# Optimization experiments

Hardware: AMD Instinct MI355X
Metric: run time of the kernel (lower is better)

The kernel has to match this reference:

```python
import jax, jax.numpy as jnp
import numpy as np

MODES1 = 32
MODES2 = 32


def _dct1_last(x):
    # Unnormalized DCT-I along last axis via rfft of even-symmetric extension.
    # For length N input, extension [x0..x_{N-1}, x_{N-2}..x_1] has length 2(N-1);
    # rfft yields N real coefficients == scipy.fftpack.dct(x, type=1).
    ext = jnp.concatenate([x, x[..., -2:0:-1]], axis=-1)
    return jnp.fft.rfft(ext, axis=-1).real.astype(x.dtype)


def _dct1_2d(x):
    # DCT-I along last two axes (separable). scipy idct type-1 (unnormalized)
    # is identical to dct type-1, so this serves as both dctn and idctn.
    x = _dct1_last(x)
    x = jnp.swapaxes(x, -1, -2)
    x = _dct1_last(x)
    return jnp.swapaxes(x, -1, -2)


def setup_inputs() -> dict:
    key = jax.random.key(0)
    k1, k2, k3 = jax.random.split(key, 3)
    B, Cin, Cout, H, W = 8, 64, 64, 256, 256
    scale = 1.0 / (Cin * Cout)
    x = jax.random.normal(k1, (B, Cin, H, W), dtype=jnp.float32)
    weights1 = scale * jax.random.uniform(k2, (Cin, Cout, MODES1, MODES2), dtype=jnp.float32)
    weights2 = scale * jax.random.uniform(k3, (Cin, Cout, MODES1, MODES2), dtype=jnp.float32)
    return {"x": x, "weights1": weights1, "weights2": weights2}


def reference(x, weights1, weights2):
    B, Cin, H, W = x.shape
    Cout = weights1.shape[1]
    Wh = W // 2 + 1  # width of truncated spectral tensor (torch used cfloat, imag==0)
    m1, m2 = MODES1, MODES2

    x_dct = _dct1_2d(x)  # [B, Cin, H, W]

    low = jnp.einsum('bixy,ioxy->boxy', x_dct[:, :, :m1, :m2], weights1)
    high = jnp.einsum('bixy,ioxy->boxy', x_dct[:, :, -m1:, :m2], weights2)

    out_ft = jnp.zeros((B, Cout, H, Wh), dtype=x.dtype)
    out_ft = out_ft.at[:, :, :m1, :m2].set(low)
    out_ft = out_ft.at[:, :, H - m1:, :m2].set(high)

    # idctn(..., type=1, shape=(H, W)) zero-pads the last axis from Wh to W,
    # then applies unnormalized IDCT-I == DCT-I along axes 2,3.
    out_full = jnp.pad(out_ft, ((0, 0), (0, 0), (0, 0), (0, W - Wh)))
    return _dct1_2d(out_full)
```

## Files before the change

kernel.cpp:

```cpp
#include <hip/hip_runtime.h>
#include <math.h>

#define OFF_AT  0
#define OFF_BMT 16384
#define OFF_CMT 24576
#define OFF_DMT 40960
#define OFF_Y   49152
#define OFF_Z   1097728

__device__ __forceinline__ float cosT(int p) {
    int r = p % 510;
    if (r > 255) r = 510 - r;
    return cosf((float)r * (3.14159265358979323846f / 255.0f));
}

__global__ __launch_bounds__(256) void init_basis(float* __restrict__ ws) {
    int idx = blockIdx.x * 256 + threadIdx.x;
    if (idx < 16384) {
        int h = idx >> 6, r = idx & 63;
        int k1 = (r < 32) ? r : r + 192;
        float we = (h == 0 || h == 255) ? 1.f : 2.f;
        ws[OFF_AT + idx] = we * cosT(k1 * h);
    } else if (idx < 24576) {
        int j = idx - 16384; int w = j >> 5, y = j & 31;
        float we = (w == 0 || w == 255) ? 1.f : 2.f;
        ws[OFF_BMT + j] = we * cosT(y * w);
    } else if (idx < 40960) {
        int j = idx - 24576; int r = j >> 8, h = j & 255;
        int k1 = (r < 32) ? r : r + 192;
        float wsl = (r == 0 || r == 63) ? 1.f : 2.f;
        ws[OFF_CMT + j] = wsl * cosT(k1 * h);
    } else if (idx < 49152) {
        int j = idx - 40960; int y = j >> 8, w = j & 255;
        float wy = (y == 0) ? 1.f : 2.f;
        ws[OFF_DMT + j] = wy * cosT(y * w);
    }
}

__global__ __launch_bounds__(256) void fwd_kernel(const float* __restrict__ x,
                                                  const float* __restrict__ ws,
                                                  float* __restrict__ Y) {
    __shared__ float buf[9216];
    __shared__ float bmt[1024];
    const int t = threadIdx.x;
    const int bi = blockIdx.x;
    const float* xp = x + (size_t)bi * 65536;
    const int l = t & 63;
    const int y8 = (t >> 6) * 8;

    float acc[4][8];
#pragma unroll
    for (int j = 0; j < 4; ++j)
#pragma unroll
        for (int yy = 0; yy < 8; ++yy) acc[j][yy] = 0.f;

    const int colv = (t & 7) * 4;
    const int rbase = t >> 3;

    for (int c = 0; c < 8; ++c) {
#pragma unroll
        for (int r = 0; r < 8; ++r) {
            int row = r * 32 + rbase;
            float4 v = *(const float4*)(xp + row * 256 + c * 32 + colv);
            float* dst = &buf[row * 33 + colv];
            dst[0] = v.x; dst[1] = v.y; dst[2] = v.z; dst[3] = v.w;
        }
        {
            int wloc = t >> 3;
            int y4 = (t & 7) * 4;
            *(float4*)&bmt[wloc * 32 + y4] =
                *(const float4*)(ws + OFF_BMT + (c * 32 + wloc) * 32 + y4);
        }
        __syncthreads();
#pragma unroll 8
        for (int w = 0; w < 32; ++w) {
            float xv0 = buf[l * 33 + w];
            float xv1 = buf[(l + 64) * 33 + w];
            float xv2 = buf[(l + 128) * 33 + w];
            float xv3 = buf[(l + 192) * 33 + w];
            float4 b0 = *(float4*)&bmt[w * 32 + y8];
            float4 b1 = *(float4*)&bmt[w * 32 + y8 + 4];
            float bv[8] = {b0.x, b0.y, b0.z, b0.w, b1.x, b1.y, b1.z, b1.w};
#pragma unroll
            for (int yy = 0; yy < 8; ++yy) {
                acc[0][yy] += xv0 * bv[yy];
                acc[1][yy] += xv1 * bv[yy];
                acc[2][yy] += xv2 * bv[yy];
                acc[3][yy] += xv3 * bv[yy];
            }
        }
        __syncthreads();
    }
#pragma unroll
    for (int j = 0; j < 4; ++j)
#pragma unroll
        for (int yy = 0; yy < 8; ++yy)
            buf[(l + 64 * j) * 36 + y8 + yy] = acc[j][yy];
    __syncthreads();

    float acc2[8];
#pragma unroll
    for (int yy = 0; yy < 8; ++yy) acc2[yy] = 0.f;
    const float* At = ws + OFF_AT;
#pragma unroll 4
    for (int h = 0; h < 256; ++h) {
        float av = At[h * 64 + l];
        float4 t0 = *(float4*)&buf[h * 36 + y8];
        float4 t1 = *(float4*)&buf[h * 36 + y8 + 4];
        acc2[0] += av * t0.x; acc2[1] += av * t0.y;
        acc2[2] += av * t0.z; acc2[3] += av * t0.w;
        acc2[4] += av * t1.x; acc2[5] += av * t1.y;
        acc2[6] += av * t1.z; acc2[7] += av * t1.w;
    }
    float* Yp = Y + (size_t)bi * 2048 + l * 32 + y8;
    *(float4*)Yp       = make_float4(acc2[0], acc2[1], acc2[2], acc2[3]);
    *(float4*)(Yp + 4) = make_float4(acc2[4], acc2[5], acc2[6], acc2[7]);
}

__global__ __launch_bounds__(256) void mix_kernel(const float* __restrict__ w1,
                                                  const float* __restrict__ w2,
                                                  const float* __restrict__ Yv,
                                                  float* __restrict__ Z) {
    const int xp = blockIdx.x & 63;
    const int o0 = (blockIdx.x >> 6) * 16;
    const int t = threadIdx.x;
    const int yh = t & 15;
    const int oo = t >> 4;
    const int o = o0 + oo;
    const int y = yh * 2;

    const float* Wbase = (xp < 32) ? (w1 + xp * 32) : (w2 + (xp - 32) * 32);
    Wbase += o * 1024 + y;
    const float* Yb = Yv + xp * 32 + y;

    float acc[8][2];
#pragma unroll
    for (int b = 0; b < 8; ++b) { acc[b][0] = 0.f; acc[b][1] = 0.f; }

    for (int i = 0; i < 64; ++i) {
        float2 wv = *(const float2*)(Wbase + i * 65536);
#pragma unroll
        for (int b = 0; b < 8; ++b) {
            float2 yv = *(const float2*)(Yb + (b * 64 + i) * 2048);
            acc[b][0] += yv.x * wv.x;
            acc[b][1] += yv.y * wv.y;
        }
    }
#pragma unroll
    for (int b = 0; b < 8; ++b) {
        float2 r; r.x = acc[b][0]; r.y = acc[b][1];
        *(float2*)(Z + (size_t)(b * 64 + o) * 2048 + xp * 32 + y) = r;
    }
}

__global__ __launch_bounds__(256) void inv_kernel(const float* __restrict__ ws,
                                                  const float* __restrict__ Zv,
                                                  float* __restrict__ out) {
    __shared__ float zs[2048];
    __shared__ float dmts[8192];
    __shared__ float t2t[4224];
    const int t = threadIdx.x;
    const int bo = blockIdx.x;
    const float* Zp = Zv + (size_t)bo * 2048;
    float* op = out + (size_t)bo * 65536;

    *(float4*)&zs[t * 8]     = *(const float4*)(Zp + t * 8);
    *(float4*)&zs[t * 8 + 4] = *(const float4*)(Zp + t * 8 + 4);
#pragma unroll
    for (int k = 0; k < 8; ++k)
        *(float4*)&dmts[k * 1024 + t * 4] =
            *(const float4*)(ws + OFF_DMT + k * 1024 + t * 4);
    __syncthreads();

    const int l6 = t & 63;
    const int y8 = (t >> 6) * 8;
    const int l5 = t & 31;
    const int j  = t >> 5;

    for (int hh = 0; hh < 2; ++hh) {
        float a1[2][8];
#pragma unroll
        for (int jj = 0; jj < 2; ++jj)
#pragma unroll
            for (int yy = 0; yy < 8; ++yy) a1[jj][yy] = 0.f;
        const float* Cm = ws + OFF_CMT + hh * 128 + l6;
#pragma unroll 4
        for (int xpi = 0; xpi < 64; ++xpi) {
            float av0 = Cm[xpi * 256];
            float av1 = Cm[xpi * 256 + 64];
            float4 z0 = *(float4*)&zs[xpi * 32 + y8];
            float4 z1 = *(float4*)&zs[xpi * 32 + y8 + 4];
            float zv[8] = {z0.x, z0.y, z0.z, z0.w, z1.x, z1.y, z1.z, z1.w};
#pragma unroll
            for (int yy = 0; yy < 8; ++yy) {
                a1[0][yy] += av0 * zv[yy];
                a1[1][yy] += av1 * zv[yy];
            }
        }
#pragma unroll
        for (int jj = 0; jj < 2; ++jj)
#pragma unroll
            for (int yy = 0; yy < 8; ++yy)
                t2t[(y8 + yy) * 132 + l6 + 64 * jj] = a1[jj][yy];
        __syncthreads();

        for (int hg = 0; hg < 2; ++hg) {
            float a2[8][8];
#pragma unroll
            for (int ii = 0; ii < 8; ++ii)
#pragma unroll
                for (int ww = 0; ww < 8; ++ww) a2[ii][ww] = 0.f;
            const int hb = hg * 64 + j * 8;
#pragma unroll 4
            for (int y = 0; y < 32; ++y) {
                float4 ta = *(float4*)&t2t[y * 132 + hb];
                float4 tb = *(float4*)&t2t[y * 132 + hb + 4];
                float4 da = *(float4*)&dmts[y * 256 + l5 * 8];
                float4 db = *(float4*)&dmts[y * 256 + l5 * 8 + 4];
                float tv[8] = {ta.x, ta.y, ta.z, ta.w, tb.x, tb.y, tb.z, tb.w};
                float dv[8] = {da.x, da.y, da.z, da.w, db.x, db.y, db.z, db.w};
#pragma unroll
                for (int ii = 0; ii < 8; ++ii)
#pragma unroll
                    for (int ww = 0; ww < 8; ++ww)
                        a2[ii][ww] += tv[ii] * dv[ww];
            }
#pragma unroll
            for (int ii = 0; ii < 8; ++ii) {
                int h = hh * 128 + hb + ii;
                float* o8 = op + h * 256 + l5 * 8;
                *(float4*)o8       = make_float4(a2[ii][0], a2[ii][1], a2[ii][2], a2[ii][3]);
                *(float4*)(o8 + 4) = make_float4(a2[ii][4], a2[ii][5], a2[ii][6], a2[ii][7]);
            }
        }
        __syncthreads();
    }
}

extern "C" void kernel_launch(void* const* d_in, const int* in_sizes, int n_in,
                              void* d_out, int out_size, void* d_ws, size_t ws_size,
                              hipStream_t stream) {
    const float* x  = (const float*)d_in[0];
    const float* w1 = (const float*)d_in[1];
    const float* w2 = (const float*)d_in[2];
    float* out = (float*)d_out;
    float* ws  = (float*)d_ws;

    hipLaunchKernelGGL(init_basis, dim3(192), dim3(256), 0, stream, ws);
    hipLaunchKernelGGL(fwd_kernel, dim3(512), dim3(256), 0, stream, x, ws, ws + OFF_Y);
    hipLaunchKernelGGL(mix_kernel, dim3(256), dim3(256), 0, stream, w1, w2,
                       ws + OFF_Y, ws + OFF_Z);
    hipLaunchKernelGGL(inv_kernel, dim3(512), dim3(256), 0, stream, ws, ws + OFF_Z, out);
}
```

Baseline: 326.8 us.

## Double-buffer forward stage, widen blocks to 512 threads, split mix work finer

The forward kernel now streams 16-column chunks of the input through double-buffered LDS with an XOR swizzle, prefetching the next chunk into registers while computing the current one, and uses 512 threads per block. The inverse kernel also moves to 512 threads, handling both h-groups in one pass instead of looping. The mix kernel is split across four times as many blocks, each thread covering two batches instead of eight, for more parallelism. This aims to raise occupancy and hide global memory latency, at the cost of less per-thread reuse and more redundant weight loads in the mix stage.

```diff
diff --git a/kernel.cpp b/kernel.cpp
--- a/kernel.cpp
+++ b/kernel.cpp
@@ -37,125 +37,129 @@
     }
 }
 
-__global__ __launch_bounds__(256) void fwd_kernel(const float* __restrict__ x,
-                                                  const float* __restrict__ ws,
-                                                  float* __restrict__ Y) {
-    __shared__ float buf[9216];
-    __shared__ float bmt[1024];
+__global__ __launch_bounds__(512, 4) void fwd_kernel(const float* __restrict__ x,
+                                                     const float* __restrict__ ws,
+                                                     float* __restrict__ Y) {
+    __shared__ float lds[9216];
     const int t = threadIdx.x;
     const int bi = blockIdx.x;
     const float* xp = x + (size_t)bi * 65536;
-    const int l = t & 63;
-    const int y8 = (t >> 6) * 8;
-
-    float acc[4][8];
-#pragma unroll
-    for (int j = 0; j < 4; ++j)
+
+    const int srow = t >> 2;
+    const int scol = (t & 3) * 4;
+    const int scolz = scol ^ (4 * ((srow >> 1) & 3));
+
+    const int hb = t & 127;
+    const int y8 = (t >> 7) * 8;
+    const int csw = 4 * ((hb >> 1) & 3);
+
+    float acc[2][8];
+#pragma unroll
+    for (int j = 0; j < 2; ++j)
 #pragma unroll
         for (int yy = 0; yy < 8; ++yy) acc[j][yy] = 0.f;
 
-    const int colv = (t & 7) * 4;
-    const int rbase = t >> 3;
-
-    for (int c = 0; c < 8; ++c) {
-#pragma unroll
-        for (int r = 0; r < 8; ++r) {
-            int row = r * 32 + rbase;
-            float4 v = *(const float4*)(xp + row * 256 + c * 32 + colv);
-            float* dst = &buf[row * 33 + colv];
-            dst[0] = v.x; dst[1] = v.y; dst[2] = v.z; dst[3] = v.w;
-        }
-        {
-            int wloc = t >> 3;
-            int y4 = (t & 7) * 4;
-            *(float4*)&bmt[wloc * 32 + y4] =
-                *(const float4*)(ws + OFF_BMT + (c * 32 + wloc) * 32 + y4);
+    float4 sx0 = *(const float4*)(xp + srow * 256 + scol);
+    float4 sx1 = *(const float4*)(xp + (srow + 128) * 256 + scol);
+    float  sb  = ws[OFF_BMT + t];
+    *(float4*)&lds[srow * 16 + scolz] = sx0;
+    *(float4*)&lds[(srow + 128) * 16 + scolz] = sx1;
+    lds[8192 + t] = sb;
+    __syncthreads();
+
+    for (int c = 0; c < 16; ++c) {
+        const int cur = c & 1;
+        if (c < 15) {
+            const int wofs = (c + 1) * 16;
+            sx0 = *(const float4*)(xp + srow * 256 + wofs + scol);
+            sx1 = *(const float4*)(xp + (srow + 128) * 256 + wofs + scol);
+            sb  = ws[OFF_BMT + (c + 1) * 512 + t];
+        }
+        const float* xs = lds + cur * 4096;
+        const float* bs = lds + 8192 + cur * 512;
+#pragma unroll
+        for (int w = 0; w < 16; w += 4) {
+            const int wz = w ^ csw;
+            float4 xa = *(const float4*)&xs[hb * 16 + wz];
+            float4 xc = *(const float4*)&xs[(hb + 128) * 16 + wz];
+            const float xav[4] = {xa.x, xa.y, xa.z, xa.w};
+            const float xcv[4] = {xc.x, xc.y, xc.z, xc.w};
+#pragma unroll
+            for (int k = 0; k < 4; ++k) {
+                float4 b0 = *(const float4*)&bs[(w + k) * 32 + y8];
+                float4 b1 = *(const float4*)&bs[(w + k) * 32 + y8 + 4];
+                const float bv[8] = {b0.x, b0.y, b0.z, b0.w, b1.x, b1.y, b1.z, b1.w};
+#pragma unroll
+                for (int yy = 0; yy < 8; ++yy) {
+                    acc[0][yy] += xav[k] * bv[yy];
+                    acc[1][yy] += xcv[k] * bv[yy];
+                }
+            }
+        }
+        if (c < 15) {
+            const int nxt = cur ^ 1;
+            *(float4*)&lds[nxt * 4096 + srow * 16 + scolz] = sx0;
+            *(float4*)&lds[nxt * 4096 + (srow + 128) * 16 + scolz] = sx1;
+            lds[8192 + nxt * 512 + t] = sb;
         }
         __syncthreads();
-#pragma unroll 8
-        for (int w = 0; w < 32; ++w) {
-            float xv0 = buf[l * 33 + w];
-            float xv1 = buf[(l + 64) * 33 + w];
-            float xv2 = buf[(l + 128) * 33 + w];
-            float xv3 = buf[(l + 192) * 33 + w];
-            float4 b0 = *(float4*)&bmt[w * 32 + y8];
-            float4 b1 = *(float4*)&bmt[w * 32 + y8 + 4];
-            float bv[8] = {b0.x, b0.y, b0.z, b0.w, b1.x, b1.y, b1.z, b1.w};
-#pragma unroll
-            for (int yy = 0; yy < 8; ++yy) {
-                acc[0][yy] += xv0 * bv[yy];
-                acc[1][yy] += xv1 * bv[yy];
-                acc[2][yy] += xv2 * bv[yy];
-                acc[3][yy] += xv3 * bv[yy];
-            }
-        }
-        __syncthreads();
-    }
-#pragma unroll
-    for (int j = 0; j < 4; ++j)
-#pragma unroll
-        for (int yy = 0; yy < 8; ++yy)
-            buf[(l + 64 * j) * 36 + y8 + yy] = acc[j][yy];
+    }
+
+#pragma unroll
+    for (int j = 0; j < 2; ++j) {
+        const int row = hb + 128 * j;
+        *(float4*)&lds[row * 36 + y8]     = make_float4(acc[j][0], acc[j][1], acc[j][2], acc[j][3]);
+        *(float4*)&lds[row * 36 + y8 + 4] = make_float4(acc[j][4], acc[j][5], acc[j][6], acc[j][7]);
+    }
     __syncthreads();
 
-    float acc2[8];
-#pragma unroll
-    for (int yy = 0; yy < 8; ++yy) acc2[yy] = 0.f;
+    const int r2 = t & 63;
+    const int y4 = (t >> 6) * 4;
+    float a2[4] = {0.f, 0.f, 0.f, 0.f};
     const float* At = ws + OFF_AT;
 #pragma unroll 4
     for (int h = 0; h < 256; ++h) {
-        float av = At[h * 64 + l];
-        float4 t0 = *(float4*)&buf[h * 36 + y8];
-        float4 t1 = *(float4*)&buf[h * 36 + y8 + 4];
-        acc2[0] += av * t0.x; acc2[1] += av * t0.y;
-        acc2[2] += av * t0.z; acc2[3] += av * t0.w;
-        acc2[4] += av * t1.x; acc2[5] += av * t1.y;
-        acc2[6] += av * t1.z; acc2[7] += av * t1.w;
-    }
-    float* Yp = Y + (size_t)bi * 2048 + l * 32 + y8;
-    *(float4*)Yp       = make_float4(acc2[0], acc2[1], acc2[2], acc2[3]);
-    *(float4*)(Yp + 4) = make_float4(acc2[4], acc2[5], acc2[6], acc2[7]);
+        const float av = At[h * 64 + r2];
+        const float4 tv = *(const float4*)&lds[h * 36 + y4];
+        a2[0] += av * tv.x; a2[1] += av * tv.y; a2[2] += av * tv.z; a2[3] += av * tv.w;
+    }
+    float* Yp = Y + (size_t)bi * 2048 + r2 * 32 + y4;
+    *(float4*)Yp = make_float4(a2[0], a2[1], a2[2], a2[3]);
 }
 
 __global__ __launch_bounds__(256) void mix_kernel(const float* __restrict__ w1,
                                                   const float* __restrict__ w2,
                                                   const float* __restrict__ Yv,
                                                   float* __restrict__ Z) {
-    const int xp = blockIdx.x & 63;
-    const int o0 = (blockIdx.x >> 6) * 16;
-    const int t = threadIdx.x;
-    const int yh = t & 15;
-    const int oo = t >> 4;
-    const int o = o0 + oo;
-    const int y = yh * 2;
-
-    const float* Wbase = (xp < 32) ? (w1 + xp * 32) : (w2 + (xp - 32) * 32);
-    Wbase += o * 1024 + y;
-    const float* Yb = Yv + xp * 32 + y;
-
-    float acc[8][2];
-#pragma unroll
-    for (int b = 0; b < 8; ++b) { acc[b][0] = 0.f; acc[b][1] = 0.f; }
-
+    const int r  = blockIdx.x & 63;
+    const int og = blockIdx.x >> 6;
+    const int t  = threadIdx.x;
+    const int y  = (t & 15) * 2;
+    const int o  = og * 4 + ((t >> 4) & 3);
+    const int bp = t >> 6;
+
+    const float* Wb = ((r < 32) ? (w1 + r * 32) : (w2 + (r - 32) * 32)) + o * 1024 + y;
+    const float* Y0 = Yv + (size_t)(bp * 64) * 2048 + r * 32 + y;
+    const float* Y1 = Y0 + (size_t)4 * 64 * 2048;
+
+    float a00 = 0.f, a01 = 0.f, a10 = 0.f, a11 = 0.f;
+#pragma unroll 4
     for (int i = 0; i < 64; ++i) {
-        float2 wv = *(const float2*)(Wbase + i * 65536);
-#pragma unroll
-        for (int b = 0; b < 8; ++b) {
-            float2 yv = *(const float2*)(Yb + (b * 64 + i) * 2048);
-            acc[b][0] += yv.x * wv.x;
-            acc[b][1] += yv.y * wv.y;
-        }
-    }
-#pragma unroll
-    for (int b = 0; b < 8; ++b) {
-        float2 r; r.x = acc[b][0]; r.y = acc[b][1];
-        *(float2*)(Z + (size_t)(b * 64 + o) * 2048 + xp * 32 + y) = r;
-    }
-}
-
-__global__ __launch_bounds__(256) void inv_kernel(const float* __restrict__ ws,
-                                                  const float* __restrict__ Zv,
-                                                  float* __restrict__ out) {
+        const float2 wv = *(const float2*)(Wb + (size_t)i * 65536);
+        const float2 p  = *(const float2*)(Y0 + i * 2048);
+        const float2 q  = *(const float2*)(Y1 + i * 2048);
+        a00 += p.x * wv.x; a01 += p.y * wv.y;
+        a10 += q.x * wv.x; a11 += q.y * wv.y;
+    }
+    float2 r0; r0.x = a00; r0.y = a01;
+    float2 r1; r1.x = a10; r1.y = a11;
+    *(float2*)(Z + (size_t)(bp * 64 + o) * 2048 + r * 32 + y) = r0;
+    *(float2*)(Z + (size_t)((bp + 4) * 64 + o) * 2048 + r * 32 + y) = r1;
+}
+
+__global__ __launch_bounds__(512, 4) void inv_kernel(const float* __restrict__ ws,
+                                                     const float* __restrict__ Zv,
+                                                     float* __restrict__ out) {
     __shared__ float zs[2048];
     __shared__ float dmts[8192];
     __shared__ float t2t[4224];
@@ -164,74 +168,66 @@
     const float* Zp = Zv + (size_t)bo * 2048;
     float* op = out + (size_t)bo * 65536;
 
-    *(float4*)&zs[t * 8]     = *(const float4*)(Zp + t * 8);
-    *(float4*)&zs[t * 8 + 4] = *(const float4*)(Zp + t * 8 + 4);
-#pragma unroll
-    for (int k = 0; k < 8; ++k)
-        *(float4*)&dmts[k * 1024 + t * 4] =
-            *(const float4*)(ws + OFF_DMT + k * 1024 + t * 4);
+    *(float4*)&zs[t * 4] = *(const float4*)(Zp + t * 4);
+#pragma unroll
+    for (int k = 0; k < 4; ++k)
+        *(float4*)&dmts[k * 2048 + t * 4] = *(const float4*)(ws + OFF_DMT + k * 2048 + t * 4);
     __syncthreads();
 
-    const int l6 = t & 63;
-    const int y8 = (t >> 6) * 8;
-    const int l5 = t & 31;
-    const int j  = t >> 5;
+    const int hb = t & 63;
+    const int y4 = (t >> 6) * 4;
+    const int wl = t & 31;
+    const int hg = t >> 5;
+    const int w0 = wl * 8;
 
     for (int hh = 0; hh < 2; ++hh) {
-        float a1[2][8];
-#pragma unroll
-        for (int jj = 0; jj < 2; ++jj)
-#pragma unroll
-            for (int yy = 0; yy < 8; ++yy) a1[jj][yy] = 0.f;
-        const float* Cm = ws + OFF_CMT + hh * 128 + l6;
+        float a1[2][4];
+#pragma unroll
+        for (int j = 0; j < 2; ++j)
+#pragma unroll
+            for (int k = 0; k < 4; ++k) a1[j][k] = 0.f;
+        const float* Cm = ws + OFF_CMT + hh * 128 + hb;
+#pragma unroll 2
+        for (int r = 0; r < 64; ++r) {
+            const float4 zv = *(const float4*)&zs[r * 32 + y4];
+            const float av0 = Cm[r * 256];
+            const float av1 = Cm[r * 256 + 64];
+            a1[0][0] += av0 * zv.x; a1[0][1] += av0 * zv.y; a1[0][2] += av0 * zv.z; a1[0][3] += av0 * zv.w;
+            a1[1][0] += av1 * zv.x; a1[1][1] += av1 * zv.y; a1[1][2] += av1 * zv.z; a1[1][3] += av1 * zv.w;
+        }
+#pragma unroll
+        for (int j = 0; j < 2; ++j)
+#pragma unroll
+            for (int k = 0; k < 4; ++k)
+                t2t[(y4 + k) * 132 + hb + 64 * j] = a1[j][k];
+        __syncthreads();
+
+        const int hbl = hg * 8;
+        float a2[8][8];
+#pragma unroll
+        for (int ii = 0; ii < 8; ++ii)
+#pragma unroll
+            for (int ww = 0; ww < 8; ++ww) a2[ii][ww] = 0.f;
 #pragma unroll 4
-        for (int xpi = 0; xpi < 64; ++xpi) {
-            float av0 = Cm[xpi * 256];
-            float av1 = Cm[xpi * 256 + 64];
-            float4 z0 = *(float4*)&zs[xpi * 32 + y8];
-            float4 z1 = *(float4*)&zs[xpi * 32 + y8 + 4];
-            float zv[8] = {z0.x, z0.y, z0.z, z0.w, z1.x, z1.y, z1.z, z1.w};
-#pragma unroll
-            for (int yy = 0; yy < 8; ++yy) {
-                a1[0][yy] += av0 * zv[yy];
-                a1[1][yy] += av1 * zv[yy];
-            }
-        }
-#pragma unroll
-        for (int jj = 0; jj < 2; ++jj)
-#pragma unroll
-            for (int yy = 0; yy < 8; ++yy)
-                t2t[(y8 + yy) * 132 + l6 + 64 * jj] = a1[jj][yy];
-        __syncthreads();
-
-        for (int hg = 0; hg < 2; ++hg) {
-            float a2[8][8];
+        for (int y = 0; y < 32; ++y) {
+            const float4 ta = *(const float4*)&t2t[y * 132 + hbl];
+            const float4 tb = *(const float4*)&t2t[y * 132 + hbl + 4];
+            const float4 da = *(const float4*)&dmts[y * 256 + w0];
+            const float4 db = *(const float4*)&dmts[y * 256 + w0 + 4];
+            const float tv[8] = {ta.x, ta.y, ta.z, ta.w, tb.x, tb.y, tb.z, tb.w};
+            const float dv[8] = {da.x, da.y, da.z, da.w, db.x, db.y, db.z, db.w};
 #pragma unroll
             for (int ii = 0; ii < 8; ++ii)
 #pragma unroll
-                for (int ww = 0; ww < 8; ++ww) a2[ii][ww] = 0.f;
-            const int hb = hg * 64 + j * 8;
-#pragma unroll 4
-            for (int y = 0; y < 32; ++y) {
-                float4 ta = *(float4*)&t2t[y * 132 + hb];
-                float4 tb = *(float4*)&t2t[y * 132 + hb + 4];
-                float4 da = *(float4*)&dmts[y * 256 + l5 * 8];
-                float4 db = *(float4*)&dmts[y * 256 + l5 * 8 + 4];
-                float tv[8] = {ta.x, ta.y, ta.z, ta.w, tb.x, tb.y, tb.z, tb.w};
-                float dv[8] = {da.x, da.y, da.z, da.w, db.x, db.y, db.z, db.w};
-#pragma unroll
-                for (int ii = 0; ii < 8; ++ii)
-#pragma unroll
-                    for (int ww = 0; ww < 8; ++ww)
-                        a2[ii][ww] += tv[ii] * dv[ww];
-            }
-#pragma unroll
-            for (int ii = 0; ii < 8; ++ii) {
-                int h = hh * 128 + hb + ii;
-                float* o8 = op + h * 256 + l5 * 8;
-                *(float4*)o8       = make_float4(a2[ii][0], a2[ii][1], a2[ii][2], a2[ii][3]);
-                *(float4*)(o8 + 4) = make_float4(a2[ii][4], a2[ii][5], a2[ii][6], a2[ii][7]);
-            }
+                for (int ww = 0; ww < 8; ++ww)
+                    a2[ii][ww] += tv[ii] * dv[ww];
+        }
+#pragma unroll
+        for (int ii = 0; ii < 8; ++ii) {
+            const int h = hh * 128 + hbl + ii;
+            float* o8 = op + h * 256 + w0;
+            *(float4*)o8       = make_float4(a2[ii][0], a2[ii][1], a2[ii][2], a2[ii][3]);
+            *(float4*)(o8 + 4) = make_float4(a2[ii][4], a2[ii][5], a2[ii][6], a2[ii][7]);
         }
         __syncthreads();
     }
@@ -247,8 +243,8 @@
     float* ws  = (float*)d_ws;
 
     hipLaunchKernelGGL(init_basis, dim3(192), dim3(256), 0, stream, ws);
-    hipLaunchKernelGGL(fwd_kernel, dim3(512), dim3(256), 0, stream, x, ws, ws + OFF_Y);
-    hipLaunchKernelGGL(mix_kernel, dim3(256), dim3(256), 0, stream, w1, w2,
+    hipLaunchKernelGGL(fwd_kernel, dim3(512), dim3(512), 0, stream, x, ws, ws + OFF_Y);
+    hipLaunchKernelGGL(mix_kernel, dim3(1024), dim3(256), 0, stream, w1, w2,
                        ws + OFF_Y, ws + OFF_Z);
-    hipLaunchKernelGGL(inv_kernel, dim3(512), dim3(256), 0, stream, ws, ws + OFF_Z, out);
-}
+    hipLaunchKernelGGL(inv_kernel, dim3(512), dim3(512), 0, stream, ws, ws + OFF_Z, out);
+}
```

After: 344.0 us. 5.3% more time.
